# Performance work log

Measured on AMD Instinct MI355X. Metric: run time of the kernel, lower is better.

Reference implementation:

```python
import jax, jax.numpy as jnp
import numpy as np

N, W, MAX_DEPTH = 250_000, 784, 16
N_NODES = 2 ** MAX_DEPTH + 1  # 65537
DEPTH = MAX_DEPTH - 1  # deepest traversal that keeps indices in-range


def setup_inputs() -> dict:
    key = jax.random.key(0)
    k1, k2, k3 = jax.random.split(key, 3)
    x = jax.random.randint(k1, (N, W), 0, 2, dtype=jnp.int32)  # binary features
    node_choices = jax.random.randint(k2, (N_NODES,), 0, W, dtype=jnp.int32)
    node_predictions = jax.random.randint(k3, (N_NODES,), 0, 2).astype(jnp.float32)
    return {"x": x, "node_choices": node_choices,
            "node_predictions": node_predictions, "depth": DEPTH}


def reference(x, node_choices, node_predictions, depth):
    # Sequential decision-tree traversal: at each level gather the split
    # feature index for every sample's current node, read that feature bit,
    # and descend to child 2*n+1 (bit=0) or 2*n+2 (bit=1).
    n = x.shape[0]
    nodes0 = jnp.zeros((n,), dtype=jnp.int32)

    def body(_, nodes):
        choices = node_choices[nodes]                                   # [n]
        decisions = jnp.take_along_axis(x, choices[:, None].astype(jnp.int32), axis=1)[:, 0]
        return nodes * 2 + decisions + 1

    nodes = jax.lax.fori_loop(0, depth, body, nodes0)
    return node_predictions[nodes].astype(jnp.bool_)
```

## Files before the change

kernel.cpp:

```cpp
#include <hip/hip_runtime.h>


#define WPR 25

__global__ __launch_bounds__(256) void fused_kernel(
    const int*   __restrict__ x,
    const int*   __restrict__ choices,
    const float* __restrict__ preds,
    const int*   __restrict__ depth_p,
    int*         __restrict__ out,
    int n)
{
    __shared__ unsigned bits[WPR * 256];

    const int tid = threadIdx.x;
    const long long r = (long long)blockIdx.x * 256 + tid;
    if (r >= n) return;

    const int4* __restrict__ rowp = (const int4*)(x + r * 784LL);

    #pragma unroll 2
    for (int ww = 0; ww < 24; ++ww) {
        unsigned a = 0;
        #pragma unroll
        for (int j = 0; j < 8; ++j) {
            const int4 v = rowp[(ww << 3) + j];
            a |= (unsigned)(v.x & 1) << ((j << 2) + 0);
            a |= (unsigned)(v.y & 1) << ((j << 2) + 1);
            a |= (unsigned)(v.z & 1) << ((j << 2) + 2);
            a |= (unsigned)(v.w & 1) << ((j << 2) + 3);
        }
        bits[ww * 256 + tid] = a;
    }
    {
        unsigned a = 0;
        #pragma unroll
        for (int j = 0; j < 4; ++j) {
            const int4 v = rowp[192 + j];
            a |= (unsigned)(v.x & 1) << ((j << 2) + 0);
            a |= (unsigned)(v.y & 1) << ((j << 2) + 1);
            a |= (unsigned)(v.z & 1) << ((j << 2) + 2);
            a |= (unsigned)(v.w & 1) << ((j << 2) + 3);
        }
        bits[24 * 256 + tid] = a;
    }

    const int depth = *depth_p;
    int node = 0;
    for (int d = 0; d < depth; ++d) {
        const int c = choices[node];
        const unsigned wv = bits[(c >> 5) * 256 + tid];
        node = (node << 1) + (int)((wv >> (c & 31)) & 1u) + 1;
    }
    out[r] = (preds[node] != 0.0f) ? 1 : 0;
}

__global__ __launch_bounds__(256) void direct_kernel(
    const int*   __restrict__ x,
    const int*   __restrict__ choices,
    const float* __restrict__ preds,
    const int*   __restrict__ depth_p,
    int*         __restrict__ out,
    int n, int w)
{
    const int i = blockIdx.x * blockDim.x + threadIdx.x;
    if (i >= n) return;
    const int depth = *depth_p;
    const int* __restrict__ row = x + (long long)i * (long long)w;
    int node = 0;
    for (int d = 0; d < depth; ++d) {
        const int c   = choices[node];
        const int bit = row[c];
        node = node * 2 + bit + 1;
    }
    out[i] = (preds[node] != 0.0f) ? 1 : 0;
}

extern "C" void kernel_launch(void* const* d_in, const int* in_sizes, int n_in,
                              void* d_out, int out_size, void* d_ws, size_t ws_size,
                              hipStream_t stream) {
    const int*   x       = (const int*)d_in[0];
    const int*   choices = (const int*)d_in[1];
    const float* preds   = (const float*)d_in[2];
    const int*   depth_p = (const int*)d_in[3];
    int*         out     = (int*)d_out;

    const int n = out_size;
    const int w = in_sizes[0] / n;

    const int block = 256;
    const int grid  = (n + block - 1) / block;

    if (w == 784) {
        fused_kernel<<<grid, block, 0, stream>>>(x, choices, preds, depth_p,
                                                 out, n);
    } else {
        direct_kernel<<<grid, block, 0, stream>>>(x, choices, preds, depth_p,
                                                  out, n, w);
    }
}
```

Measured before the change: 1.012 ms.

## Coalesce row loads per wavefront and pack bits with ballot

Each wavefront now loads whole rows cooperatively, each lane reading consecutive int4s, so the 784-int rows are read with coalesced accesses instead of one row per thread with strided loads. Feature bits are packed into 32-bit words with __ballot in a permuted bit layout, and lanes 0/1 write them to shared memory. The traversal recomputes word and bit indices for the new layout. This adds many ballot operations and scattered shared-memory stores, and clamps out-of-range rows to the last row.

```diff
diff --git a/kernel.cpp b/kernel.cpp
--- a/kernel.cpp
+++ b/kernel.cpp
@@ -1,7 +1,7 @@
 #include <hip/hip_runtime.h>
 
 
-#define WPR 25
+#define WPR 28
 
 __global__ __launch_bounds__(256) void fused_kernel(
     const int*   __restrict__ x,
@@ -13,46 +13,70 @@
 {
     __shared__ unsigned bits[WPR * 256];
 
-    const int tid = threadIdx.x;
-    const long long r = (long long)blockIdx.x * 256 + tid;
-    if (r >= n) return;
+    const int tid  = threadIdx.x;
+    const int lane = tid & 63;
+    const int wid  = tid >> 6;
+    const long long base = (long long)blockIdx.x * 256;
 
-    const int4* __restrict__ rowp = (const int4*)(x + r * 784LL);
+    for (int it = 0; it < 16; ++it) {
+        const int r0 = (wid << 6) + (it << 2);
 
-    #pragma unroll 2
-    for (int ww = 0; ww < 24; ++ww) {
-        unsigned a = 0;
+        int4 v0[4], v1[4], v2[4], v3[4];
         #pragma unroll
-        for (int j = 0; j < 8; ++j) {
-            const int4 v = rowp[(ww << 3) + j];
-            a |= (unsigned)(v.x & 1) << ((j << 2) + 0);
-            a |= (unsigned)(v.y & 1) << ((j << 2) + 1);
-            a |= (unsigned)(v.z & 1) << ((j << 2) + 2);
-            a |= (unsigned)(v.w & 1) << ((j << 2) + 3);
+        for (int rr = 0; rr < 4; ++rr) {
+            long long gr = base + r0 + rr;
+            if (gr >= n) gr = n - 1;
+            const int4* __restrict__ rowp = (const int4*)(x + gr * 784LL);
+            v0[rr] = rowp[lane];
+            v1[rr] = rowp[64 + lane];
+            v2[rr] = rowp[128 + lane];
+            v3[rr] = rowp[192 + (lane & 3)];
         }
-        bits[ww * 256 + tid] = a;
+
+        #pragma unroll
+        for (int rr = 0; rr < 4; ++rr) {
+            const int col = r0 + rr;
+            unsigned long long m[12];
+            #pragma unroll
+            for (int cmp = 0; cmp < 4; ++cmp) {
+                m[0 + cmp] = __ballot(((&v0[rr].x)[cmp] & 1) != 0);
+                m[4 + cmp] = __ballot(((&v1[rr].x)[cmp] & 1) != 0);
+                m[8 + cmp] = __ballot(((&v2[rr].x)[cmp] & 1) != 0);
+            }
+            unsigned long long t[4];
+            #pragma unroll
+            for (int cmp = 0; cmp < 4; ++cmp)
+                t[cmp] = __ballot(((&v3[rr].x)[cmp] & 1) != 0);
+
+            if (lane < 2) {
+                #pragma unroll
+                for (int q = 0; q < 12; ++q) {
+                    const int w = ((q >> 2) << 3) + ((q & 3) << 1) + lane;
+                    bits[w * 256 + col] = (unsigned)(m[q] >> (lane << 5));
+                }
+            }
+            if (lane == 0) {
+                #pragma unroll
+                for (int cmp = 0; cmp < 4; ++cmp)
+                    bits[(24 + cmp) * 256 + col] = (unsigned)t[cmp];
+            }
+        }
     }
-    {
-        unsigned a = 0;
-        #pragma unroll
-        for (int j = 0; j < 4; ++j) {
-            const int4 v = rowp[192 + j];
-            a |= (unsigned)(v.x & 1) << ((j << 2) + 0);
-            a |= (unsigned)(v.y & 1) << ((j << 2) + 1);
-            a |= (unsigned)(v.z & 1) << ((j << 2) + 2);
-            a |= (unsigned)(v.w & 1) << ((j << 2) + 3);
-        }
-        bits[24 * 256 + tid] = a;
-    }
+
+    const long long i = base + tid;
+    if (i >= n) return;
 
     const int depth = *depth_p;
     int node = 0;
     for (int d = 0; d < depth; ++d) {
-        const int c = choices[node];
-        const unsigned wv = bits[(c >> 5) * 256 + tid];
-        node = (node << 1) + (int)((wv >> (c & 31)) & 1u) + 1;
+        const int c  = choices[node];
+        int w;
+        if (c < 768) w = ((c >> 8) << 3) | ((c & 3) << 1) | ((c >> 7) & 1);
+        else         w = 24 | (c & 3);
+        const unsigned wv = bits[w * 256 + tid];
+        node = (node << 1) + (int)((wv >> ((c >> 2) & 31)) & 1u) + 1;
     }
-    out[r] = (preds[node] != 0.0f) ? 1 : 0;
+    out[i] = (preds[node] != 0.0f) ? 1 : 0;
 }
 
 __global__ __launch_bounds__(256) void direct_kernel(
```

Result: faster. 978.3 us (-3.4%).
